# Optimization experiments

Hardware: AMD Instinct MI355X
Metric: run time of the kernel (lower is better)

Reference implementation:

```python
import jax, jax.numpy as jnp
import numpy as np
import math

S, B, D, H = 2048, 2, 1024, 16
DK = D // H

def setup_inputs() -> dict:
    key = jax.random.key(0)
    ks = jax.random.split(key, 32)
    f = lambda k, shape, s=1.0: jax.random.normal(k, shape, dtype=jnp.float32) * s
    inp = {
        'qx': f(ks[0], (S, B, D)),
        'kx': f(ks[1], (S, B, D)),
        'vx': f(ks[2], (S, B, D)),
        'qc': f(ks[3], (S, B, D)),
        'kc': f(ks[4], (S, B, D)),
    }
    w = 1.0 / math.sqrt(D)
    names = ['qx_lin', 'kx_lin', 'vx_lin', 'qc_lin', 'kc_lin', 'out_lin']
    for i, n in enumerate(names):
        inp['W_' + n] = f(ks[5 + 2 * i], (D, D), w)
        inp['b_' + n] = f(ks[6 + 2 * i], (D,), w)
    vnames = ['Vqx', 'Vqc', 'Vkx', 'Vkc']
    for i, n in enumerate(vnames):
        inp['W_' + n] = f(ks[17 + 2 * i], (D, 1), w)
        inp['b_' + n] = f(ks[18 + 2 * i], (1,), w)
    return inp

def _forward(qx, kx, vx, qc, kc,
             W_qx_lin, b_qx_lin, W_kx_lin, b_kx_lin, W_vx_lin, b_vx_lin,
             W_qc_lin, b_qc_lin, W_kc_lin, b_kc_lin, W_out_lin, b_out_lin,
             W_Vqx, b_Vqx, W_Vqc, b_Vqc, W_Vkx, b_Vkx, W_Vkc, b_Vkc):
    # [S,B,D] -> [B,S,D]
    qx = jnp.swapaxes(qx, 0, 1)
    kx = jnp.swapaxes(kx, 0, 1)
    vx = jnp.swapaxes(vx, 0, 1)
    qc = jnp.swapaxes(qc, 0, 1)
    kc = jnp.swapaxes(kc, 0, 1)
    bs = qx.shape[0]

    qx = qx @ W_qx_lin + b_qx_lin
    kx = kx @ W_kx_lin + b_kx_lin
    v = vx @ W_vx_lin + b_vx_lin
    qc = qc @ W_qc_lin + b_qc_lin
    kc = kc @ W_kc_lin + b_kc_lin

    lam_q = jax.nn.sigmoid((qx @ W_Vqx + b_Vqx) + (qc @ W_Vqc + b_Vqc))  # [B,S,1]
    lam_k = jax.nn.sigmoid((kx @ W_Vkx + b_Vkx) + (kc @ W_Vkc + b_Vkc))
    q = (1.0 - lam_q) * qx + lam_q * qc
    k = (1.0 - lam_k) * kx + lam_k * kc

    # [B,S,D] -> [B,H,S,dk]
    q = q.reshape(bs, -1, H, DK).transpose(0, 2, 1, 3)
    k = k.reshape(bs, -1, H, DK).transpose(0, 2, 1, 3)
    v = v.reshape(bs, -1, H, DK).transpose(0, 2, 1, 3)

    scores = jnp.einsum('bhqd,bhkd->bhqk', q, k) / math.sqrt(DK)
    attn = jax.nn.softmax(scores, axis=-1)  # dropout is identity in eval
    ctx = jnp.einsum('bhqk,bhkd->bhqd', attn, v)

    concat = ctx.transpose(0, 2, 1, 3).reshape(bs, -1, D)
    out = concat @ W_out_lin + b_out_lin
    return jnp.swapaxes(out, 0, 1)  # back to [S,B,D]

def reference(qx, kx, vx, qc, kc,
              W_qx_lin, b_qx_lin, W_kx_lin, b_kx_lin, W_vx_lin, b_vx_lin,
              W_qc_lin, b_qc_lin, W_kc_lin, b_kc_lin, W_out_lin, b_out_lin,
              W_Vqx, b_Vqx, W_Vqc, b_Vqc, W_Vkx, b_Vkx, W_Vkc, b_Vkc):
    return _forward(qx, kx, vx, qc, kc,
                    W_qx_lin, b_qx_lin, W_kx_lin, b_kx_lin, W_vx_lin, b_vx_lin,
                    W_qc_lin, b_qc_lin, W_kc_lin, b_kc_lin, W_out_lin, b_out_lin,
                    W_Vqx, b_Vqx, W_Vqc, b_Vqc, W_Vkx, b_Vkx, W_Vkc, b_Vkc)
```

## Files before the change

kernel.cpp:

```cpp
#include <hip/hip_runtime.h>
#include <math.h>

typedef unsigned short u16;
typedef __attribute__((ext_vector_type(8))) short short8;
typedef __attribute__((ext_vector_type(4))) float floatx4;
typedef __attribute__((ext_vector_type(4))) unsigned short ushort4v;
typedef __attribute__((ext_vector_type(2))) unsigned int uint2v;

__device__ __forceinline__ float bf2f(u16 x) {
    union { unsigned int u; float f; } v; v.u = ((unsigned int)x) << 16; return v.f;
}
__device__ __forceinline__ u16 f2bf(float f) {
    union { float f; unsigned int u; } v; v.f = f;
    unsigned int r = v.u + 0x7fffu + ((v.u >> 16) & 1u);
    return (u16)(r >> 16);
}
__device__ __forceinline__ unsigned int pk2bf(float a, float b) {
#if __has_builtin(__builtin_amdgcn_cvt_pk_bf16_f32)
    auto r = __builtin_amdgcn_cvt_pk_bf16_f32(a, b);
    union { decltype(r) v; unsigned int u; } cv; cv.v = r; return cv.u;
#else
    return (unsigned int)f2bf(a) | ((unsigned int)f2bf(b) << 16);
#endif
}
__device__ __forceinline__ float fexp2(float x) {
#if __has_builtin(__builtin_amdgcn_exp2f)
    return __builtin_amdgcn_exp2f(x);
#else
    return exp2f(x);
#endif
}

__device__ __forceinline__ void swap32(unsigned int& x0, unsigned int& x1, int lane) {
#if __has_builtin(__builtin_amdgcn_permlane32_swap)
    (void)lane;
    auto r = __builtin_amdgcn_permlane32_swap((int)x0, (int)x1, false, false);
    x0 = (unsigned int)r[0]; x1 = (unsigned int)r[1];
#else
    const bool hi = (lane & 32) != 0;
    const unsigned int s = hi ? x0 : x1;
    const unsigned int rr = (unsigned int)__shfl_xor((int)s, 32, 64);
    const unsigned int n0 = hi ? rr : x0;
    const unsigned int n1 = hi ? x1 : rr;
    x0 = n0; x1 = n1;
#endif
}
__device__ __forceinline__ void swap16(unsigned int& x0, unsigned int& x1, int lane) {
#if __has_builtin(__builtin_amdgcn_permlane16_swap)
    (void)lane;
    auto r = __builtin_amdgcn_permlane16_swap((int)x0, (int)x1, false, false);
    x0 = (unsigned int)r[0]; x1 = (unsigned int)r[1];
#else
    const bool hi = (lane & 16) != 0;
    const unsigned int s = hi ? x0 : x1;
    const unsigned int rr = (unsigned int)__shfl_xor((int)s, 16, 64);
    const unsigned int n0 = hi ? rr : x0;
    const unsigned int n1 = hi ? x1 : rr;
    x0 = n0; x1 = n1;
#endif
}

__device__ __forceinline__ void g2l16(const u16* g, u16* l) {
    __builtin_amdgcn_global_load_lds(
        (const __attribute__((address_space(1))) void*)g,
        (__attribute__((address_space(3))) void*)l, 16, 0, 0);
}

struct WFuseJobs { const float* W[4]; const float* wv[4]; const float* bl[4];
                   float* out[4]; float* bdot; };

__global__ __launch_bounds__(256) void wfuse(WFuseJobs wf) {
    const int z = blockIdx.y;
    const float* W = wf.W[z];
    const float* wv = wf.wv[z];
    float* out = wf.out[z];
    const int t = threadIdx.x;
    const int lane = t & 63, w = t >> 6;
#pragma unroll
    for (int i = 0; i < 4; i++) {
        const int row = blockIdx.x * 16 + w * 4 + i;
        const float* Wr = W + (size_t)row * 1024 + lane * 16;
        const float* vr = wv + lane * 16;
        float p = 0.f;
#pragma unroll
        for (int c = 0; c < 4; c++) {
            const floatx4 a = *(const floatx4*)(Wr + c * 4);
            const floatx4 b = *(const floatx4*)(vr + c * 4);
            p += a[0] * b[0] + a[1] * b[1] + a[2] * b[2] + a[3] * b[3];
        }
#pragma unroll
        for (int m = 1; m <= 32; m <<= 1) p += __shfl_xor(p, m);
        if (lane == 0) out[row] = p;
    }
    if (blockIdx.x == 0) {
        const floatx4 bb = *(const floatx4*)(wf.bl[z] + t * 4);
        const floatx4 vv = *(const floatx4*)(wv + t * 4);
        float p = bb[0] * vv[0] + bb[1] * vv[1] + bb[2] * vv[2] + bb[3] * vv[3];
#pragma unroll
        for (int m = 1; m <= 32; m <<= 1) p += __shfl_xor(p, m);
        __shared__ float red[4];
        if ((t & 63) == 0) red[t >> 6] = p;
        __syncthreads();
        if (t == 0) wf.bdot[z] = red[0] + red[1] + red[2] + red[3];
    }
}

struct GCJobs {
    const float* xa[3]; const float* xc[3];
    const float* w1[3]; const float* w2[3];
    const float* bdot;
    const float* sA[3]; const float* sB[3];
    float* lamout[3];
    u16* dst[3];
};

__global__ __launch_bounds__(256) void gatecast(GCJobs gj) {
    const int z = blockIdx.y;
    const int t = threadIdx.x;
    const int lane = t & 63, w = t >> 6;
    const int row = blockIdx.x * 4 + w;
    const int e0 = lane * 4;

    if (z == 2) {
#pragma unroll
        for (int c = 0; c < 4; c++) {
            const floatx4 a = *(const floatx4*)(gj.xa[2] + (size_t)row * 1024 + c * 256 + e0);
            ushort4v o;
            const unsigned int lo = pk2bf(a[0], a[1]);
            const unsigned int hi = pk2bf(a[2], a[3]);
            o[0] = (u16)(lo & 0xffff); o[1] = (u16)(lo >> 16);
            o[2] = (u16)(hi & 0xffff); o[3] = (u16)(hi >> 16);
            *(ushort4v*)(gj.dst[2] + (size_t)row * 1024 + c * 256 + e0) = o;
        }
        return;
    }

    floatx4 av[4], cv[4];
    float p = 0.f;
#pragma unroll
    for (int c = 0; c < 4; c++) {
        av[c] = *(const floatx4*)(gj.xa[z] + (size_t)row * 1024 + c * 256 + e0);
        cv[c] = *(const floatx4*)(gj.xc[z] + (size_t)row * 1024 + c * 256 + e0);
        const floatx4 w1 = *(const floatx4*)(gj.w1[z] + c * 256 + e0);
        const floatx4 w2 = *(const floatx4*)(gj.w2[z] + c * 256 + e0);
#pragma unroll
        for (int j = 0; j < 4; j++) p += av[c][j] * w1[j] + cv[c][j] * w2[j];
    }
#pragma unroll
    for (int m = 1; m <= 32; m <<= 1) p += __shfl_xor(p, m);
    const float x = p + gj.bdot[2 * z] + gj.bdot[2 * z + 1]
                  + gj.sA[z][0] + gj.sB[z][0];
    const float lam = 1.f / (1.f + exp2f(-x * 1.44269504f));
    if (lane == 0) gj.lamout[z][row] = lam;
    const float oml = 1.f - lam;

    u16* d = gj.dst[z] + (size_t)row * 2048;
#pragma unroll
    for (int c = 0; c < 4; c++) {
        ushort4v o1, o2;
        {
            const unsigned int lo = pk2bf(oml * av[c][0], oml * av[c][1]);
            const unsigned int hi = pk2bf(oml * av[c][2], oml * av[c][3]);
            o1[0] = (u16)(lo & 0xffff); o1[1] = (u16)(lo >> 16);
            o1[2] = (u16)(hi & 0xffff); o1[3] = (u16)(hi >> 16);
        }
        {
            const unsigned int lo = pk2bf(lam * cv[c][0], lam * cv[c][1]);
            const unsigned int hi = pk2bf(lam * cv[c][2], lam * cv[c][3]);
            o2[0] = (u16)(lo & 0xffff); o2[1] = (u16)(lo >> 16);
            o2[2] = (u16)(hi & 0xffff); o2[3] = (u16)(hi >> 16);
        }
        *(ushort4v*)(d + c * 256 + e0) = o1;
        *(ushort4v*)(d + 1024 + c * 256 + e0) = o2;
    }
}

struct WTJobs { const float* src[6]; u16* dst[6]; int stride[6]; int koff[6]; };

__global__ __launch_bounds__(256) void wtrans(WTJobs wj) {
    __shared__ float tile[32][33];
    const int z = blockIdx.z;
    const float* W = wj.src[z];
    u16* Wt = wj.dst[z];
    const int stride = wj.stride[z], koff = wj.koff[z];
    const int n0 = blockIdx.x * 32, k0 = blockIdx.y * 32;
    const int tx = threadIdx.x & 31, ty = threadIdx.x >> 5;
#pragma unroll
    for (int i = 0; i < 4; i++)
        tile[ty + i * 8][tx] = W[(size_t)(k0 + ty + i * 8) * 1024 + n0 + tx];
    __syncthreads();
#pragma unroll
    for (int i = 0; i < 4; i++)
        Wt[(size_t)(n0 + ty + i * 8) * stride + koff + k0 + tx] = f2bf(tile[tx][ty + i * 8]);
}

__global__ __launch_bounds__(256) void vtrans(const u16* __restrict__ V,
                                              u16* __restrict__ Vtg) {
    __shared__ u16 tile[32][34];
    const int bh = blockIdx.z, b = bh >> 4, h = bh & 15;
    const int base = b * 1024 + h * 64;
    const int s0 = blockIdx.x * 32, d0 = blockIdx.y * 32;
    const int tx = threadIdx.x & 31, ty = threadIdx.x >> 5;
#pragma unroll
    for (int i = 0; i < 4; i++)
        tile[ty + i * 8][tx] = V[(size_t)(s0 + ty + i * 8) * 2048 + base + d0 + tx];
    __syncthreads();
#pragma unroll
    for (int i = 0; i < 4; i++)
        Vtg[((size_t)bh * 64 + d0 + ty + i * 8) * 2048 + s0 + tx] = tile[tx][ty + i * 8];
}

struct PJob {
    const u16* A; const u16* Bt; int K;
    const float* biasA; const float* biasC; const float* lam;
    u16* out; float* outf; float scale;
};
struct PJobs { PJob j[4]; };

__global__ __launch_bounds__(256, 3) void projall(PJobs jobs) {
    __shared__ __align__(16) u16 As[2][128 * 32];
    __shared__ __align__(16) u16 Bs[2][128 * 32];
    const int nj = gridDim.z;
    const int bid = blockIdx.x + 8 * (blockIdx.y + 32 * blockIdx.z);
    const int sw = (bid & 7) * (32 * nj) + (bid >> 3);
    const PJob jb = jobs.j[sw >> 8];
    const int K = jb.K;
    const int m0 = ((sw >> 3) & 31) * 128;
    const int n0 = (sw & 7) * 128;
    const int t = threadIdx.x;
    const int lane = t & 63;
    const int wid = t >> 6;
    const int wm = wid >> 1, wn = wid & 1;
    const int qd = lane >> 4, lm = lane & 15;

    const floatx4 zero4 = {0.f, 0.f, 0.f, 0.f};
    floatx4 acc[4][4];
#pragma unroll
    for (int i = 0; i < 4; i++)
#pragma unroll
        for (int j2 = 0; j2 < 4; j2++) acc[i][j2] = zero4;

    const int srow = t >> 2;
    const int su = (t & 3) ^ (srow & 3);
    const u16* Ap = jb.A + (size_t)(m0 + srow) * K + su * 8;
    const u16* Bp = jb.Bt + (size_t)(n0 + srow) * K + su * 8;

#define PSTAGE(BUF, KOFF) do {                                         \
        g2l16(Ap + (KOFF),                   &As[BUF][t * 8]);         \
        g2l16(Ap + (KOFF) + (size_t)64 * K,  &As[BUF][2048 + t * 8]);  \
        g2l16(Bp + (KOFF),                   &Bs[BUF][t * 8]);         \
        g2l16(Bp + (KOFF) + (size_t)64 * K,  &Bs[BUF][2048 + t * 8]);  \
    } while (0)

    PSTAGE(0, 0);
    __syncthreads();
    int cur = 0;
    const int ua = (qd ^ (lm & 3)) << 3;
    for (int k0 = 0; k0 < K; k0 += 32) {
        if (k0 + 32 < K) PSTAGE(cur ^ 1, k0 + 32);

        short8 af[4], bfg[4];
#pragma unroll
        for (int i = 0; i < 4; i++) {
            af[i]  = *(const short8*)&As[cur][(wm * 64 + i * 16 + lm) * 32 + ua];
            bfg[i] = *(const short8*)&Bs[cur][(wn * 64 + i * 16 + lm) * 32 + ua];
        }
#pragma unroll
        for (int i = 0; i < 4; i++)
#pragma unroll
            for (int j2 = 0; j2 < 4; j2++)
                acc[i][j2] = __builtin_amdgcn_mfma_f32_16x16x32_bf16(af[i], bfg[j2], acc[i][j2], 0, 0, 0);

        __syncthreads();
        cur ^= 1;
    }
#undef PSTAGE

#pragma unroll
    for (int i = 0; i < 4; i++) {
        const int mb = m0 + wm * 64 + i * 16 + qd * 4;
        float lamv[4];
        if (jb.lam) {
#pragma unroll
            for (int r = 0; r < 4; r++) lamv[r] = jb.lam[mb + r];
        }
#pragma unroll
        for (int j2 = 0; j2 < 4; j2++) {
            const int col = n0 + wn * 64 + j2 * 16 + lm;
            const float bA = jb.biasA[col];
            if (jb.outf) {
#pragma unroll
                for (int r = 0; r < 4; r++)
                    jb.outf[(size_t)(mb + r) * 1024 + col] = acc[i][j2][r] + bA;
            } else if (jb.lam) {
                const float dB = jb.biasC[col] - bA;
#pragma unroll
                for (int r = 0; r < 4; r++)
                    jb.out[(size_t)(mb + r) * 1024 + col] =
                        f2bf((acc[i][j2][r] + bA + lamv[r] * dB) * jb.scale);
            } else {
#pragma unroll
                for (int r = 0; r < 4; r++)
                    jb.out[(size_t)(mb + r) * 1024 + col] =
                        f2bf((acc[i][j2][r] + bA) * jb.scale);
            }
        }
    }
}

__global__ __launch_bounds__(256, 2) void projout(const u16* __restrict__ A,
                                                  const u16* __restrict__ Bt,
                                                  const float* __restrict__ bias,
                                                  float* __restrict__ C) {
    __shared__ __align__(16) u16 As[2][128 * 32];
    __shared__ __align__(16) u16 Bs[2][64 * 32];
    const int K = 1024;
    const int bid = blockIdx.x;
    const int sw = (bid & 7) * 64 + (bid >> 3);
    const int m0 = (sw >> 4) * 128;
    const int n0 = (sw & 15) * 64;
    const int t = threadIdx.x;
    const int lane = t & 63;
    const int wid = t >> 6;
    const int wm = wid >> 1, wn = wid & 1;
    const int qd = lane >> 4, lm = lane & 15;

    const floatx4 zero4 = {0.f, 0.f, 0.f, 0.f};
    floatx4 acc[4][2];
#pragma unroll
    for (int i = 0; i < 4; i++)
#pragma unroll
        for (int j2 = 0; j2 < 2; j2++) acc[i][j2] = zero4;

    const int srow = t >> 2;
    const int su = (t & 3) ^ (srow & 3);
    const u16* Ap = A + (size_t)(m0 + srow) * K + su * 8;
    const u16* Bp = Bt + (size_t)(n0 + srow) * K + su * 8;

#define OSTG(BUF, KOFF) do {                                           \
        g2l16(Ap + (KOFF),                   &As[BUF][t * 8]);         \
        g2l16(Ap + (KOFF) + (size_t)64 * K,  &As[BUF][2048 + t * 8]);  \
        g2l16(Bp + (KOFF),                   &Bs[BUF][t * 8]);         \
    } while (0)

    OSTG(0, 0);
    __syncthreads();
    int cur = 0;
    const int ua = (qd ^ (lm & 3)) << 3;
    for (int k0 = 0; k0 < K; k0 += 32) {
        if (k0 + 32 < K) OSTG(cur ^ 1, k0 + 32);

        short8 af[4], bfg[2];
#pragma unroll
        for (int i = 0; i < 4; i++)
            af[i] = *(const short8*)&As[cur][(wm * 64 + i * 16 + lm) * 32 + ua];
#pragma unroll
        for (int j2 = 0; j2 < 2; j2++)
            bfg[j2] = *(const short8*)&Bs[cur][(wn * 32 + j2 * 16 + lm) * 32 + ua];
#pragma unroll
        for (int i = 0; i < 4; i++)
#pragma unroll
            for (int j2 = 0; j2 < 2; j2++)
                acc[i][j2] = __builtin_amdgcn_mfma_f32_16x16x32_bf16(af[i], bfg[j2], acc[i][j2], 0, 0, 0);

        __syncthreads();
        cur ^= 1;
    }
#undef OSTG

#pragma unroll
    for (int i = 0; i < 4; i++) {
        const int mb = m0 + wm * 64 + i * 16 + qd * 4;
#pragma unroll
        for (int j2 = 0; j2 < 2; j2++) {
            const int col = n0 + wn * 32 + j2 * 16 + lm;
            const float bv = bias[col];
#pragma unroll
            for (int r = 0; r < 4; r++)
                C[(size_t)(mb + r) * 1024 + col] = acc[i][j2][r] + bv;
        }
    }
}

__global__ __launch_bounds__(256, 4) void attn6(
    const u16* __restrict__ Q, const u16* __restrict__ Kk,
    const u16* __restrict__ Vtg, float* __restrict__ ctxp,
    float* __restrict__ lp) {
    __shared__ __align__(16) u16 SB[16384];

    const int bid = blockIdx.x + 16 * (blockIdx.y + 32 * blockIdx.z);
    const int sw = (bid & 7) * 128 + (bid >> 3);
    const int qt = sw & 15;
    const int bh = (sw >> 4) & 31;
    const int sp = sw >> 9;
    const int b = bh >> 4, h = bh & 15;
    const int hb = b * 1024 + h * 64;

    const int t = threadIdx.x, lane = t & 63, w = t >> 6;
    const int qd = lane >> 4, lm = lane & 15;
    const int q0w = qt * 128 + w * 32;

    short8 qf[2][2];
#pragma unroll
    for (int qh = 0; qh < 2; qh++) {
        const u16* qr = Q + (size_t)(q0w + qh * 16 + lm) * 2048 + hb;
#pragma unroll
        for (int c = 0; c < 2; c++)
            qf[qh][c] = *(const short8*)(qr + c * 32 + qd * 8);
    }

    const floatx4 zero4 = {0.f, 0.f, 0.f, 0.f};
    floatx4 ctx[2][4];
#pragma unroll
    for (int qh = 0; qh < 2; qh++)
#pragma unroll
        for (int g = 0; g < 4; g++) ctx[qh][g] = zero4;
    floatx4 accL[2] = {zero4, zero4};

    union { unsigned int u[4]; short8 s; } ov;
    ov.u[0] = ov.u[1] = ov.u[2] = ov.u[3] = 0x3F803F80u;
    const short8 onesb = ov.s;

    const int rl = lane >> 3;
    const int cuz = (lane & 7) ^ rl;
    const u16* kp = Kk + (size_t)(sp * 1024 + w * 16 + rl) * 2048 + hb + cuz * 8;
    const u16* vp = Vtg + ((size_t)bh * 64 + w * 16 + rl) * 2048 + sp * 1024 + cuz * 8;
    u16* kd = &SB[(w * 16) * 64];
    u16* vd = &SB[4096 + (w * 16) * 64];

    const int rdA = lm * 64 + ((qd ^ (lm & 7)) << 3);
    const int rdB = rdA ^ 32;

#define STAGE(BUF) do {                                             \
        g2l16(kp,            kd + (BUF) * 8192);                    \
        g2l16(kp + 8 * 2048, kd + (BUF) * 8192 + 8 * 64);           \
        g2l16(vp,            vd + (BUF) * 8192);                    \
        g2l16(vp + 8 * 2048, vd + (BUF) * 8192 + 8 * 64);           \
        kp += 64 * 2048; vp += 64;                                  \
    } while (0)

#define COMPUTE(BUF) do {                                                          \
        short8 pa[2][2];                                                           \
        _Pragma("unroll")                                                          \
        for (int gp = 0; gp < 2; gp++) {                                           \
            unsigned int pw[2][2][2];                                              \
            _Pragma("unroll")                                                      \
            for (int g0 = 0; g0 < 2; g0++) {                                       \
                const int g = gp * 2 + g0;                                         \
                const short8 kf0 = *(const short8*)&SB[(BUF) * 8192 + g * 1024 + rdA]; \
                const short8 kf1 = *(const short8*)&SB[(BUF) * 8192 + g * 1024 + rdB]; \
                _Pragma("unroll")                                                  \
                for (int qh = 0; qh < 2; qh++) {                                   \
                    floatx4 st = zero4;                                            \
                    st = __builtin_amdgcn_mfma_f32_16x16x32_bf16(kf0, qf[qh][0], st, 0, 0, 0); \
                    st = __builtin_amdgcn_mfma_f32_16x16x32_bf16(kf1, qf[qh][1], st, 0, 0, 0); \
                    const float e0 = fexp2(st[0]), e1 = fexp2(st[1]);              \
                    const float e2 = fexp2(st[2]), e3 = fexp2(st[3]);              \
                    pw[qh][g0][0] = pk2bf(e0, e1);                                 \
                    pw[qh][g0][1] = pk2bf(e2, e3);                                 \
                }                                                                  \
            }                                                                      \
            _Pragma("unroll")                                                      \
            for (int qh = 0; qh < 2; qh++) {                                       \
                unsigned int a0 = pw[qh][0][0], b0 = pw[qh][1][0];                 \
                unsigned int a1 = pw[qh][0][1], b1 = pw[qh][1][1];                 \
                swap32(a0, b0, lane); swap32(a1, b1, lane);                        \
                swap16(a0, b0, lane); swap16(a1, b1, lane);                        \
                union { unsigned int u[4]; short8 s; } cv;                         \
                cv.u[0] = a0; cv.u[1] = a1; cv.u[2] = b0; cv.u[3] = b1;            \
                pa[qh][gp] = cv.s;                                                 \
            }                                                                      \
        }                                                                          \
        __builtin_amdgcn_s_setprio(1);                                             \
        _Pragma("unroll")                                                          \
        for (int g = 0; g < 4; g++) {                                              \
            const short8 vb0 = *(const short8*)&SB[(BUF) * 8192 + 4096 + g * 1024 + rdA]; \
            const short8 vb1 = *(const short8*)&SB[(BUF) * 8192 + 4096 + g * 1024 + rdB]; \
            _Pragma("unroll")                                                      \
            for (int qh = 0; qh < 2; qh++) {                                       \
                ctx[qh][g] = __builtin_amdgcn_mfma_f32_16x16x32_bf16(pa[qh][0], vb0, ctx[qh][g], 0, 0, 0); \
                ctx[qh][g] = __builtin_amdgcn_mfma_f32_16x16x32_bf16(pa[qh][1], vb1, ctx[qh][g], 0, 0, 0); \
            }                                                                      \
        }                                                                          \
        _Pragma("unroll")                                                          \
        for (int qh = 0; qh < 2; qh++) {                                           \
            accL[qh] = __builtin_amdgcn_mfma_f32_16x16x32_bf16(pa[qh][0], onesb, accL[qh], 0, 0, 0); \
            accL[qh] = __builtin_amdgcn_mfma_f32_16x16x32_bf16(pa[qh][1], onesb, accL[qh], 0, 0, 0); \
        }                                                                          \
        __builtin_amdgcn_s_setprio(0);                                             \
    } while (0)

    STAGE(0);
#pragma unroll 1
    for (int it = 0; it < 8; it++) {
        __syncthreads();
        STAGE(1);
        COMPUTE(0);
        __syncthreads();
        if (it < 7) STAGE(0);
        COMPUTE(1);
    }
#undef STAGE
#undef COMPUTE

    float* cbase = ctxp + (size_t)sp * 4194304;
#pragma unroll
    for (int qh = 0; qh < 2; qh++) {
        if (lm == 0) {
#pragma unroll
            for (int r = 0; r < 4; r++)
                lp[(size_t)sp * 65536 + bh * 2048 + q0w + qh * 16 + qd * 4 + r] = accL[qh][r];
        }
#pragma unroll
        for (int r = 0; r < 4; r++) {
            const int srow = q0w + qh * 16 + qd * 4 + r;
            float* orow = cbase + (size_t)srow * 2048 + hb;
#pragma unroll
            for (int g = 0; g < 4; g++)
                orow[g * 16 + lm] = ctx[qh][g][r];
        }
    }
}

__global__ __launch_bounds__(256) void merge(const float* __restrict__ ctxp,
                                             const float* __restrict__ lp,
                                             u16* __restrict__ out) {
    const size_t idx = ((size_t)blockIdx.x * 256 + threadIdx.x) * 4;
    const floatx4 a = *(const floatx4*)(ctxp + idx);
    const floatx4 c = *(const floatx4*)(ctxp + 4194304 + idx);
    const int srow = (int)(idx >> 11);
    const int rem = (int)(idx & 2047);
    const int bh = rem >> 6;
    const float l = lp[bh * 2048 + srow] + lp[65536 + bh * 2048 + srow];
    const float inv = 1.0f / l;
    ushort4v o;
    const unsigned int lo = pk2bf((a[0] + c[0]) * inv, (a[1] + c[1]) * inv);
    const unsigned int hi = pk2bf((a[2] + c[2]) * inv, (a[3] + c[3]) * inv);
    o[0] = (u16)(lo & 0xffff); o[1] = (u16)(lo >> 16);
    o[2] = (u16)(hi & 0xffff); o[3] = (u16)(hi >> 16);
    *(ushort4v*)(out + idx) = o;
}

extern "C" void kernel_launch(void* const* d_in, const int* in_sizes, int n_in,
                              void* d_out, int out_size, void* d_ws, size_t ws_size,
                              hipStream_t stream) {
    const float* qx = (const float*)d_in[0];
    const float* kx = (const float*)d_in[1];
    const float* vx = (const float*)d_in[2];
    const float* qc = (const float*)d_in[3];
    const float* kc = (const float*)d_in[4];
    const float* W_qx = (const float*)d_in[5];   const float* b_qx = (const float*)d_in[6];
    const float* W_kx = (const float*)d_in[7];   const float* b_kx = (const float*)d_in[8];
    const float* W_vx = (const float*)d_in[9];   const float* b_vx = (const float*)d_in[10];
    const float* W_qc = (const float*)d_in[11];  const float* b_qc = (const float*)d_in[12];
    const float* W_kc = (const float*)d_in[13];  const float* b_kc = (const float*)d_in[14];
    const float* W_out = (const float*)d_in[15]; const float* b_out = (const float*)d_in[16];
    const float* W_Vqx = (const float*)d_in[17]; const float* b_Vqx = (const float*)d_in[18];
    const float* W_Vqc = (const float*)d_in[19]; const float* b_Vqc = (const float*)d_in[20];
    const float* W_Vkx = (const float*)d_in[21]; const float* b_Vkx = (const float*)d_in[22];
    const float* W_Vkc = (const float*)d_in[23]; const float* b_Vkc = (const float*)d_in[24];

    char* ws = (char*)d_ws;
    const size_t MB = 1048576;
    u16* Aq  = (u16*)ws;
    u16* Ak  = (u16*)(ws + 16 * MB);
    u16* Av  = (u16*)(ws + 32 * MB);
    u16* Wtq = (u16*)(ws + 40 * MB);
    u16* Wtk = (u16*)(ws + 44 * MB);
    u16* Wtv = (u16*)(ws + 48 * MB);
    u16* Wto = (u16*)(ws + 50 * MB);
    u16* Pv    = (u16*)(ws + 52 * MB);
    u16* qg    = (u16*)(ws + 60 * MB);
    u16* kg    = (u16*)(ws + 68 * MB);
    u16* ctxbf = (u16*)(ws + 76 * MB);
    float* wfused = (float*)(ws + 84 * MB);
    float* bdot   = (float*)(ws + 84 * MB + 16384);
    float* lam    = (float*)(ws + 84 * MB + 16384 + 256);
    float* l_part = (float*)(ws + 84 * MB + 16384 + 256 + 32768);
    float* ctxp = (float*)ws;
    u16* Vtg    = (u16*)(ws + 32 * MB);

    WFuseJobs wf;
    wf.W[0] = W_qx; wf.wv[0] = W_Vqx; wf.bl[0] = b_qx; wf.out[0] = wfused;
    wf.W[1] = W_qc; wf.wv[1] = W_Vqc; wf.bl[1] = b_qc; wf.out[1] = wfused + 1024;
    wf.W[2] = W_kx; wf.wv[2] = W_Vkx; wf.bl[2] = b_kx; wf.out[2] = wfused + 2048;
    wf.W[3] = W_kc; wf.wv[3] = W_Vkc; wf.bl[3] = b_kc; wf.out[3] = wfused + 3072;
    wf.bdot = bdot;
    wfuse<<<dim3(64, 4), 256, 0, stream>>>(wf);

    GCJobs gj;
    gj.xa[0] = qx; gj.xc[0] = qc; gj.w1[0] = wfused;        gj.w2[0] = wfused + 1024;
    gj.sA[0] = b_Vqx; gj.sB[0] = b_Vqc; gj.lamout[0] = lam;        gj.dst[0] = Aq;
    gj.xa[1] = kx; gj.xc[1] = kc; gj.w1[1] = wfused + 2048; gj.w2[1] = wfused + 3072;
    gj.sA[1] = b_Vkx; gj.sB[1] = b_Vkc; gj.lamout[1] = lam + 4096; gj.dst[1] = Ak;
    gj.xa[2] = vx; gj.xc[2] = nullptr; gj.w1[2] = nullptr; gj.w2[2] = nullptr;
    gj.sA[2] = nullptr; gj.sB[2] = nullptr; gj.lamout[2] = nullptr; gj.dst[2] = Av;
    gj.bdot = bdot;
    gatecast<<<dim3(1024, 3), 256, 0, stream>>>(gj);

    WTJobs wj;
    wj.src[0] = W_qx; wj.dst[0] = Wtq; wj.stride[0] = 2048; wj.koff[0] = 0;
    wj.src[1] = W_qc; wj.dst[1] = Wtq; wj.stride[1] = 2048; wj.koff[1] = 1024;
    wj.src[2] = W_kx; wj.dst[2] = Wtk; wj.stride[2] = 2048; wj.koff[2] = 0;
    wj.src[3] = W_kc; wj.dst[3] = Wtk; wj.stride[3] = 2048; wj.koff[3] = 1024;
    wj.src[4] = W_vx; wj.dst[4] = Wtv; wj.stride[4] = 1024; wj.koff[4] = 0;
    wj.src[5] = W_out; wj.dst[5] = Wto; wj.stride[5] = 1024; wj.koff[5] = 0;
    wtrans<<<dim3(32, 32, 6), 256, 0, stream>>>(wj);

    const float QSCALE = 0.18033688011112042f;
    PJobs pj;
    pj.j[0].A = Aq; pj.j[0].Bt = Wtq; pj.j[0].K = 2048;
    pj.j[0].biasA = b_qx; pj.j[0].biasC = b_qc; pj.j[0].lam = lam;
    pj.j[0].out = qg; pj.j[0].outf = nullptr; pj.j[0].scale = QSCALE;
    pj.j[1].A = Ak; pj.j[1].Bt = Wtk; pj.j[1].K = 2048;
    pj.j[1].biasA = b_kx; pj.j[1].biasC = b_kc; pj.j[1].lam = lam + 4096;
    pj.j[1].out = kg; pj.j[1].outf = nullptr; pj.j[1].scale = 1.0f;
    pj.j[2].A = Av; pj.j[2].Bt = Wtv; pj.j[2].K = 1024;
    pj.j[2].biasA = b_vx; pj.j[2].biasC = nullptr; pj.j[2].lam = nullptr;
    pj.j[2].out = Pv; pj.j[2].outf = nullptr; pj.j[2].scale = 1.0f;
    pj.j[3] = pj.j[2];
    projall<<<dim3(8, 32, 3), 256, 0, stream>>>(pj);

    vtrans<<<dim3(64, 2, 32), 256, 0, stream>>>(Pv, Vtg);

    attn6<<<dim3(16, 32, 2), 256, 0, stream>>>(qg, kg, Vtg, ctxp, l_part);

    merge<<<4096, 256, 0, stream>>>(ctxp, l_part, ctxbf);

    projout<<<dim3(512), 256, 0, stream>>>(ctxbf, Wto, b_out, (float*)d_out);
}
```

Before: 332.2 us.

## Drop split-K attention and merge pass; fuse weight transpose into gate kernel

The attention kernel no longer splits the key sequence in two. Each block now covers 64 queries (16 per wave) over the full 2048 keys and writes normalized bf16 context directly, so the separate merge kernel and its fp32 partial buffers go away. The weight-transpose kernel is folded into the gate/cast kernel as extra grid rows, which saves one launch. The cost is fewer queries per wave, so each K/V tile loaded into LDS is reused less, and each block runs twice as many iterations.

```diff
diff --git a/kernel.cpp b/kernel.cpp
--- a/kernel.cpp
+++ b/kernel.cpp
@@ -5,11 +5,7 @@
 typedef __attribute__((ext_vector_type(8))) short short8;
 typedef __attribute__((ext_vector_type(4))) float floatx4;
 typedef __attribute__((ext_vector_type(4))) unsigned short ushort4v;
-typedef __attribute__((ext_vector_type(2))) unsigned int uint2v;
-
-__device__ __forceinline__ float bf2f(u16 x) {
-    union { unsigned int u; float f; } v; v.u = ((unsigned int)x) << 16; return v.f;
-}
+
 __device__ __forceinline__ u16 f2bf(float f) {
     union { float f; unsigned int u; } v; v.f = f;
     unsigned int r = v.u + 0x7fffu + ((v.u >> 16) & 1u);
@@ -105,18 +101,38 @@
     }
 }
 
-struct GCJobs {
+struct GCWJobs {
     const float* xa[3]; const float* xc[3];
     const float* w1[3]; const float* w2[3];
     const float* bdot;
     const float* sA[3]; const float* sB[3];
     float* lamout[3];
     u16* dst[3];
+    const float* wsrc[6]; u16* wdst[6]; int wstride[6]; int wkoff[6];
 };
 
-__global__ __launch_bounds__(256) void gatecast(GCJobs gj) {
+__global__ __launch_bounds__(256) void gatewt(GCWJobs gj) {
+    __shared__ float tile[32][33];
     const int z = blockIdx.y;
     const int t = threadIdx.x;
+
+    if (z >= 3) {
+        const int j = z - 3;
+        const float* W = gj.wsrc[j];
+        u16* Wt = gj.wdst[j];
+        const int stride = gj.wstride[j], koff = gj.wkoff[j];
+        const int n0 = (blockIdx.x & 31) * 32, k0 = (blockIdx.x >> 5) * 32;
+        const int tx = t & 31, ty = t >> 5;
+#pragma unroll
+        for (int i = 0; i < 4; i++)
+            tile[ty + i * 8][tx] = W[(size_t)(k0 + ty + i * 8) * 1024 + n0 + tx];
+        __syncthreads();
+#pragma unroll
+        for (int i = 0; i < 4; i++)
+            Wt[(size_t)(n0 + ty + i * 8) * stride + koff + k0 + tx] = f2bf(tile[tx][ty + i * 8]);
+        return;
+    }
+
     const int lane = t & 63, w = t >> 6;
     const int row = blockIdx.x * 4 + w;
     const int e0 = lane * 4;
@@ -173,25 +189,6 @@
         *(ushort4v*)(d + c * 256 + e0) = o1;
         *(ushort4v*)(d + 1024 + c * 256 + e0) = o2;
     }
-}
-
-struct WTJobs { const float* src[6]; u16* dst[6]; int stride[6]; int koff[6]; };
-
-__global__ __launch_bounds__(256) void wtrans(WTJobs wj) {
-    __shared__ float tile[32][33];
-    const int z = blockIdx.z;
-    const float* W = wj.src[z];
-    u16* Wt = wj.dst[z];
-    const int stride = wj.stride[z], koff = wj.koff[z];
-    const int n0 = blockIdx.x * 32, k0 = blockIdx.y * 32;
-    const int tx = threadIdx.x & 31, ty = threadIdx.x >> 5;
-#pragma unroll
-    for (int i = 0; i < 4; i++)
-        tile[ty + i * 8][tx] = W[(size_t)(k0 + ty + i * 8) * 1024 + n0 + tx];
-    __syncthreads();
-#pragma unroll
-    for (int i = 0; i < 4; i++)
-        Wt[(size_t)(n0 + ty + i * 8) * stride + koff + k0 + tx] = f2bf(tile[tx][ty + i * 8]);
 }
 
 __global__ __launch_bounds__(256) void vtrans(const u16* __restrict__ V,
@@ -382,40 +379,34 @@
     }
 }
 
-__global__ __launch_bounds__(256, 4) void attn6(
+__global__ __launch_bounds__(256, 4) void attn7(
     const u16* __restrict__ Q, const u16* __restrict__ Kk,
-    const u16* __restrict__ Vtg, float* __restrict__ ctxp,
-    float* __restrict__ lp) {
+    const u16* __restrict__ Vtg, u16* __restrict__ ctxbf) {
     __shared__ __align__(16) u16 SB[16384];
 
-    const int bid = blockIdx.x + 16 * (blockIdx.y + 32 * blockIdx.z);
+    const int bid = blockIdx.x + 32 * blockIdx.y;
     const int sw = (bid & 7) * 128 + (bid >> 3);
-    const int qt = sw & 15;
-    const int bh = (sw >> 4) & 31;
-    const int sp = sw >> 9;
+    const int qt = sw & 31;
+    const int bh = sw >> 5;
     const int b = bh >> 4, h = bh & 15;
     const int hb = b * 1024 + h * 64;
 
     const int t = threadIdx.x, lane = t & 63, w = t >> 6;
     const int qd = lane >> 4, lm = lane & 15;
-    const int q0w = qt * 128 + w * 32;
-
-    short8 qf[2][2];
-#pragma unroll
-    for (int qh = 0; qh < 2; qh++) {
-        const u16* qr = Q + (size_t)(q0w + qh * 16 + lm) * 2048 + hb;
-#pragma unroll
-        for (int c = 0; c < 2; c++)
-            qf[qh][c] = *(const short8*)(qr + c * 32 + qd * 8);
+    const int q0w = qt * 64 + w * 16;
+
+    short8 qf[2];
+    {
+        const u16* qr = Q + (size_t)(q0w + lm) * 2048 + hb;
+        qf[0] = *(const short8*)(qr + qd * 8);
+        qf[1] = *(const short8*)(qr + 32 + qd * 8);
     }
 
     const floatx4 zero4 = {0.f, 0.f, 0.f, 0.f};
-    floatx4 ctx[2][4];
-#pragma unroll
-    for (int qh = 0; qh < 2; qh++)
-#pragma unroll
-        for (int g = 0; g < 4; g++) ctx[qh][g] = zero4;
-    floatx4 accL[2] = {zero4, zero4};
+    floatx4 ctx[4];
+#pragma unroll
+    for (int g = 0; g < 4; g++) ctx[g] = zero4;
+    floatx4 accL = zero4;
 
     union { unsigned int u[4]; short8 s; } ov;
     ov.u[0] = ov.u[1] = ov.u[2] = ov.u[3] = 0x3F803F80u;
@@ -423,8 +414,8 @@
 
     const int rl = lane >> 3;
     const int cuz = (lane & 7) ^ rl;
-    const u16* kp = Kk + (size_t)(sp * 1024 + w * 16 + rl) * 2048 + hb + cuz * 8;
-    const u16* vp = Vtg + ((size_t)bh * 64 + w * 16 + rl) * 2048 + sp * 1024 + cuz * 8;
+    const u16* kp = Kk + (size_t)(w * 16 + rl) * 2048 + hb + cuz * 8;
+    const u16* vp = Vtg + ((size_t)bh * 64 + w * 16 + rl) * 2048 + cuz * 8;
     u16* kd = &SB[(w * 16) * 64];
     u16* vd = &SB[4096 + (w * 16) * 64];
 
@@ -440,105 +431,66 @@
     } while (0)
 
 #define COMPUTE(BUF) do {                                                          \
-        short8 pa[2][2];                                                           \
+        short8 pa[2];                                                              \
         _Pragma("unroll")                                                          \
         for (int gp = 0; gp < 2; gp++) {                                           \
-            unsigned int pw[2][2][2];                                              \
+            unsigned int pw[2][2];                                                 \
             _Pragma("unroll")                                                      \
             for (int g0 = 0; g0 < 2; g0++) {                                       \
                 const int g = gp * 2 + g0;                                         \
                 const short8 kf0 = *(const short8*)&SB[(BUF) * 8192 + g * 1024 + rdA]; \
                 const short8 kf1 = *(const short8*)&SB[(BUF) * 8192 + g * 1024 + rdB]; \
-                _Pragma("unroll")                                                  \
-                for (int qh = 0; qh < 2; qh++) {                                   \
-                    floatx4 st = zero4;                                            \
-                    st = __builtin_amdgcn_mfma_f32_16x16x32_bf16(kf0, qf[qh][0], st, 0, 0, 0); \
-                    st = __builtin_amdgcn_mfma_f32_16x16x32_bf16(kf1, qf[qh][1], st, 0, 0, 0); \
-                    const float e0 = fexp2(st[0]), e1 = fexp2(st[1]);              \
-                    const float e2 = fexp2(st[2]), e3 = fexp2(st[3]);              \
-                    pw[qh][g0][0] = pk2bf(e0, e1);                                 \
-                    pw[qh][g0][1] = pk2bf(e2, e3);                                 \
-                }                                                                  \
+                floatx4 st = zero4;                                                \
+                st = __builtin_amdgcn_mfma_f32_16x16x32_bf16(kf0, qf[0], st, 0, 0, 0); \
+                st = __builtin_amdgcn_mfma_f32_16x16x32_bf16(kf1, qf[1], st, 0, 0, 0); \
+                const float e0 = fexp2(st[0]), e1 = fexp2(st[1]);                  \
+                const float e2 = fexp2(st[2]), e3 = fexp2(st[3]);                  \
+                pw[g0][0] = pk2bf(e0, e1);                                         \
+                pw[g0][1] = pk2bf(e2, e3);                                         \
             }                                                                      \
-            _Pragma("unroll")                                                      \
-            for (int qh = 0; qh < 2; qh++) {                                       \
-                unsigned int a0 = pw[qh][0][0], b0 = pw[qh][1][0];                 \
-                unsigned int a1 = pw[qh][0][1], b1 = pw[qh][1][1];                 \
-                swap32(a0, b0, lane); swap32(a1, b1, lane);                        \
-                swap16(a0, b0, lane); swap16(a1, b1, lane);                        \
-                union { unsigned int u[4]; short8 s; } cv;                         \
-                cv.u[0] = a0; cv.u[1] = a1; cv.u[2] = b0; cv.u[3] = b1;            \
-                pa[qh][gp] = cv.s;                                                 \
-            }                                                                      \
+            unsigned int a0 = pw[0][0], b0 = pw[1][0];                             \
+            unsigned int a1 = pw[0][1], b1 = pw[1][1];                             \
+            swap32(a0, b0, lane); swap32(a1, b1, lane);                            \
+            swap16(a0, b0, lane); swap16(a1, b1, lane);                            \
+            union { unsigned int u[4]; short8 s; } cvv;                            \
+            cvv.u[0] = a0; cvv.u[1] = a1; cvv.u[2] = b0; cvv.u[3] = b1;            \
+            pa[gp] = cvv.s;                                                        \
         }                                                                          \
         __builtin_amdgcn_s_setprio(1);                                             \
         _Pragma("unroll")                                                          \
         for (int g = 0; g < 4; g++) {                                              \
             const short8 vb0 = *(const short8*)&SB[(BUF) * 8192 + 4096 + g * 1024 + rdA]; \
             const short8 vb1 = *(const short8*)&SB[(BUF) * 8192 + 4096 + g * 1024 + rdB]; \
-            _Pragma("unroll")                                                      \
-            for (int qh = 0; qh < 2; qh++) {                                       \
-                ctx[qh][g] = __builtin_amdgcn_mfma_f32_16x16x32_bf16(pa[qh][0], vb0, ctx[qh][g], 0, 0, 0); \
-                ctx[qh][g] = __builtin_amdgcn_mfma_f32_16x16x32_bf16(pa[qh][1], vb1, ctx[qh][g], 0, 0, 0); \
-            }                                                                      \
+            ctx[g] = __builtin_amdgcn_mfma_f32_16x16x32_bf16(pa[0], vb0, ctx[g], 0, 0, 0); \
+            ctx[g] = __builtin_amdgcn_mfma_f32_16x16x32_bf16(pa[1], vb1, ctx[g], 0, 0, 0); \
         }                                                                          \
-        _Pragma("unroll")                                                          \
-        for (int qh = 0; qh < 2; qh++) {                                           \
-            accL[qh] = __builtin_amdgcn_mfma_f32_16x16x32_bf16(pa[qh][0], onesb, accL[qh], 0, 0, 0); \
-            accL[qh] = __builtin_amdgcn_mfma_f32_16x16x32_bf16(pa[qh][1], onesb, accL[qh], 0, 0, 0); \
-        }                                                                          \
+        accL = __builtin_amdgcn_mfma_f32_16x16x32_bf16(pa[0], onesb, accL, 0, 0, 0); \
+        accL = __builtin_amdgcn_mfma_f32_16x16x32_bf16(pa[1], onesb, accL, 0, 0, 0); \
         __builtin_amdgcn_s_setprio(0);                                             \
     } while (0)
 
     STAGE(0);
 #pragma unroll 1
-    for (int it = 0; it < 8; it++) {
+    for (int it = 0; it < 16; it++) {
         __syncthreads();
         STAGE(1);
         COMPUTE(0);
         __syncthreads();
-        if (it < 7) STAGE(0);
+        if (it < 15) STAGE(0);
         COMPUTE(1);
     }
 #undef STAGE
 #undef COMPUTE
 
-    float* cbase = ctxp + (size_t)sp * 4194304;
-#pragma unroll
-    for (int qh = 0; qh < 2; qh++) {
-        if (lm == 0) {
-#pragma unroll
-            for (int r = 0; r < 4; r++)
-                lp[(size_t)sp * 65536 + bh * 2048 + q0w + qh * 16 + qd * 4 + r] = accL[qh][r];
-        }
-#pragma unroll
-        for (int r = 0; r < 4; r++) {
-            const int srow = q0w + qh * 16 + qd * 4 + r;
-            float* orow = cbase + (size_t)srow * 2048 + hb;
-#pragma unroll
-            for (int g = 0; g < 4; g++)
-                orow[g * 16 + lm] = ctx[qh][g][r];
-        }
-    }
-}
-
-__global__ __launch_bounds__(256) void merge(const float* __restrict__ ctxp,
-                                             const float* __restrict__ lp,
-                                             u16* __restrict__ out) {
-    const size_t idx = ((size_t)blockIdx.x * 256 + threadIdx.x) * 4;
-    const floatx4 a = *(const floatx4*)(ctxp + idx);
-    const floatx4 c = *(const floatx4*)(ctxp + 4194304 + idx);
-    const int srow = (int)(idx >> 11);
-    const int rem = (int)(idx & 2047);
-    const int bh = rem >> 6;
-    const float l = lp[bh * 2048 + srow] + lp[65536 + bh * 2048 + srow];
-    const float inv = 1.0f / l;
-    ushort4v o;
-    const unsigned int lo = pk2bf((a[0] + c[0]) * inv, (a[1] + c[1]) * inv);
-    const unsigned int hi = pk2bf((a[2] + c[2]) * inv, (a[3] + c[3]) * inv);
-    o[0] = (u16)(lo & 0xffff); o[1] = (u16)(lo >> 16);
-    o[2] = (u16)(hi & 0xffff); o[3] = (u16)(hi >> 16);
-    *(ushort4v*)(out + idx) = o;
+#pragma unroll
+    for (int r = 0; r < 4; r++) {
+        const float inv = 1.0f / accL[r];
+        const int srow = q0w + qd * 4 + r;
+        u16* orow = ctxbf + (size_t)srow * 2048 + hb;
+#pragma unroll
+        for (int g = 0; g < 4; g++)
+            orow[g * 16 + lm] = f2bf(ctx[g][r] * inv);
+    }
 }
 
 extern "C" void kernel_launch(void* const* d_in, const int* in_sizes, int n_in,
@@ -576,8 +528,6 @@
     float* wfused = (float*)(ws + 84 * MB);
     float* bdot   = (float*)(ws + 84 * MB + 16384);
     float* lam    = (float*)(ws + 84 * MB + 16384 + 256);
-    float* l_part = (float*)(ws + 84 * MB + 16384 + 256 + 32768);
-    float* ctxp = (float*)ws;
     u16* Vtg    = (u16*)(ws + 32 * MB);
 
     WFuseJobs wf;
@@ -588,7 +538,7 @@
     wf.bdot = bdot;
     wfuse<<<dim3(64, 4), 256, 0, stream>>>(wf);
 
-    GCJobs gj;
+    GCWJobs gj;
     gj.xa[0] = qx; gj.xc[0] = qc; gj.w1[0] = wfused;        gj.w2[0] = wfused + 1024;
     gj.sA[0] = b_Vqx; gj.sB[0] = b_Vqc; gj.lamout[0] = lam;        gj.dst[0] = Aq;
     gj.xa[1] = kx; gj.xc[1] = kc; gj.w1[1] = wfused + 2048; gj.w2[1] = wfused + 3072;
@@ -596,16 +546,13 @@
     gj.xa[2] = vx; gj.xc[2] = nullptr; gj.w1[2] = nullptr; gj.w2[2] = nullptr;
     gj.sA[2] = nullptr; gj.sB[2] = nullptr; gj.lamout[2] = nullptr; gj.dst[2] = Av;
     gj.bdot = bdot;
-    gatecast<<<dim3(1024, 3), 256, 0, stream>>>(gj);
-
-    WTJobs wj;
-    wj.src[0] = W_qx; wj.dst[0] = Wtq; wj.stride[0] = 2048; wj.koff[0] = 0;
-    wj.src[1] = W_qc; wj.dst[1] = Wtq; wj.stride[1] = 2048; wj.koff[1] = 1024;
-    wj.src[2] = W_kx; wj.dst[2] = Wtk; wj.stride[2] = 2048; wj.koff[2] = 0;
-    wj.src[3] = W_kc; wj.dst[3] = Wtk; wj.stride[3] = 2048; wj.koff[3] = 1024;
-    wj.src[4] = W_vx; wj.dst[4] = Wtv; wj.stride[4] = 1024; wj.koff[4] = 0;
-    wj.src[5] = W_out; wj.dst[5] = Wto; wj.stride[5] = 1024; wj.koff[5] = 0;
-    wtrans<<<dim3(32, 32, 6), 256, 0, stream>>>(wj);
+    gj.wsrc[0] = W_qx; gj.wdst[0] = Wtq; gj.wstride[0] = 2048; gj.wkoff[0] = 0;
+    gj.wsrc[1] = W_qc; gj.wdst[1] = Wtq; gj.wstride[1] = 2048; gj.wkoff[1] = 1024;
+    gj.wsrc[2] = W_kx; gj.wdst[2] = Wtk; gj.wstride[2] = 2048; gj.wkoff[2] = 0;
+    gj.wsrc[3] = W_kc; gj.wdst[3] = Wtk; gj.wstride[3] = 2048; gj.wkoff[3] = 1024;
+    gj.wsrc[4] = W_vx; gj.wdst[4] = Wtv; gj.wstride[4] = 1024; gj.wkoff[4] = 0;
+    gj.wsrc[5] = W_out; gj.wdst[5] = Wto; gj.wstride[5] = 1024; gj.wkoff[5] = 0;
+    gatewt<<<dim3(1024, 9), 256, 0, stream>>>(gj);
 
     const float QSCALE = 0.18033688011112042f;
     PJobs pj;
@@ -623,9 +570,7 @@
 
     vtrans<<<dim3(64, 2, 32), 256, 0, stream>>>(Pv, Vtg);
 
-    attn6<<<dim3(16, 32, 2), 256, 0, stream>>>(qg, kg, Vtg, ctxp, l_part);
-
-    merge<<<4096, 256, 0, stream>>>(ctxp, l_part, ctxbf);
+    attn7<<<dim3(32, 32), 256, 0, stream>>>(qg, kg, Vtg, ctxbf);
 
     projout<<<dim3(512), 256, 0, stream>>>(ctxbf, Wto, b_out, (float*)d_out);
 }
```

Result: no change. 332.4 us (+0.1%).
